# Kernel tuning notes

Hardware: AMD Instinct MI355X
Metric: run time of the kernel (lower is better)

## Reference

```python
import jax, jax.numpy as jnp
import numpy as np

N = 50000      # nodes
E = 800000     # edges (before self-loops)
IN = 128       # in_channels
HID = 32       # hidden_channels
H = 4          # heads (hidden layers)
H_LAST = 6     # heads of final conv (concat=False -> mean)
OUT = 2        # out_channels
NEG = 0.2      # LeakyReLU slope in GATConv


def setup_inputs() -> dict:
    key = jax.random.key(0)
    ks = jax.random.split(key, 24)
    r = lambda k, s, sc=0.1: (jax.random.normal(k, s, jnp.float32) * sc)
    inp = {
        "x": jax.random.normal(ks[0], (N, IN), jnp.float32),
        "edge_index": jax.random.randint(ks[1], (2, E), 0, N, dtype=jnp.int32),
        "edge_attr": jax.random.normal(ks[2], (E, 1), jnp.float32),  # ignored by GATConv (edge_dim=None)
        # layer 0: GATConv(IN -> HID, heads=H, concat) + Linear(IN -> HID*H)
        "c0_W": r(ks[3], (IN, H * HID)), "c0_as": r(ks[4], (H, HID)), "c0_ad": r(ks[5], (H, HID)), "c0_b": jnp.zeros((H * HID,), jnp.float32),
        "l0_W": r(ks[6], (IN, H * HID)), "l0_b": jnp.zeros((H * HID,), jnp.float32),
        # layer 1 (middle): GATConv(HID*H -> HID, heads=H) + Linear(HID*H -> HID*H)
        "c1_W": r(ks[7], (H * HID, H * HID)), "c1_as": r(ks[8], (H, HID)), "c1_ad": r(ks[9], (H, HID)), "c1_b": jnp.zeros((H * HID,), jnp.float32),
        "l1_W": r(ks[10], (H * HID, H * HID)), "l1_b": jnp.zeros((H * HID,), jnp.float32),
        # layer 2 (last): GATConv(HID*H -> OUT, heads=H_LAST, concat=False) + Linear(HID*H -> OUT)
        "c2_W": r(ks[11], (H * HID, H_LAST * OUT)), "c2_as": r(ks[12], (H_LAST, OUT)), "c2_ad": r(ks[13], (H_LAST, OUT)), "c2_b": jnp.zeros((OUT,), jnp.float32),
        "l2_W": r(ks[14], (H * HID, OUT)), "l2_b": jnp.zeros((OUT,), jnp.float32),
    }
    return inp


def gat_conv(x, src, dst, W, a_src, a_dst, b, heads, ch, concat):
    n = x.shape[0]
    xw = (x @ W).reshape(n, heads, ch)                      # [N,H,C]
    al_s = jnp.einsum('nhc,hc->nh', xw, a_src)              # [N,H]
    al_d = jnp.einsum('nhc,hc->nh', xw, a_dst)
    alpha = jax.nn.leaky_relu(al_s[src] + al_d[dst], NEG)   # [E,H]
    # segment softmax over edges sharing the same destination node
    m = jax.ops.segment_max(alpha, dst, num_segments=n)
    e = jnp.exp(alpha - m[dst])
    s = jax.ops.segment_sum(e, dst, num_segments=n)
    coef = e / s[dst]                                       # [E,H]
    out = jax.ops.segment_sum(xw[src] * coef[:, :, None], dst, num_segments=n)  # [N,H,C]
    out = out.reshape(n, heads * ch) if concat else out.mean(axis=1)
    return out + b


def reference(x, edge_index, edge_attr,
              c0_W, c0_as, c0_ad, c0_b, l0_W, l0_b,
              c1_W, c1_as, c1_ad, c1_b, l1_W, l1_b,
              c2_W, c2_as, c2_ad, c2_b, l2_W, l2_b):
    n = x.shape[0]
    loops = jnp.arange(n, dtype=edge_index.dtype)  # GATConv add_self_loops=True
    src = jnp.concatenate([edge_index[0], loops])
    dst = jnp.concatenate([edge_index[1], loops])
    # edge_attr is ignored: GATConv built without edge_dim has lin_edge=None
    h = jax.nn.relu(gat_conv(x, src, dst, c0_W, c0_as, c0_ad, c0_b, H, HID, True) + x @ l0_W + l0_b)
    h = jax.nn.relu(gat_conv(h, src, dst, c1_W, c1_as, c1_ad, c1_b, H, HID, True) + h @ l1_W + l1_b)
    out = gat_conv(h, src, dst, c2_W, c2_as, c2_ad, c2_b, H_LAST, OUT, False) + h @ l2_W + l2_b
    return out
```

## Files before the change

kernel.cpp:

```cpp
#include <hip/hip_runtime.h>
#include <hip/hip_bf16.h>


#define NEG_SLOPE 0.2f
#define SC_CHUNK 4096
#define CAP 64
#define CSTR 16

typedef __attribute__((ext_vector_type(8))) short short8;
typedef __attribute__((ext_vector_type(4))) float floatx4;

static __device__ __forceinline__ float leaky(float x) {
    return x > 0.f ? x : NEG_SLOPE * x;
}

static __device__ __forceinline__ unsigned short f2bf(float f) {
    unsigned int u = __float_as_uint(f);
    u = (u + 0x7fffu + ((u >> 16) & 1u)) >> 16;
    return (unsigned short)u;
}

static __device__ __forceinline__ unsigned int pack_bf2(float lo, float hi) {
    return (unsigned int)f2bf(lo) | ((unsigned int)f2bf(hi) << 16);
}

static __device__ __forceinline__ float bflo(unsigned int u) {
    return __uint_as_float(u << 16);
}
static __device__ __forceinline__ float bfhi(unsigned int u) {
    return __uint_as_float(u & 0xffff0000u);
}

static __device__ __forceinline__ short8 frag_from_f32(const float* p) {
    float4 f0 = ((const float4*)p)[0];
    float4 f1 = ((const float4*)p)[1];
    short8 r;
    r[0] = (short)f2bf(f0.x); r[1] = (short)f2bf(f0.y);
    r[2] = (short)f2bf(f0.z); r[3] = (short)f2bf(f0.w);
    r[4] = (short)f2bf(f1.x); r[5] = (short)f2bf(f1.y);
    r[6] = (short)f2bf(f1.z); r[7] = (short)f2bf(f1.w);
    return r;
}

__global__ __launch_bounds__(256) void k_bucket(
    const int* __restrict__ ei, int E, int N, int rs,
    int* __restrict__ cnt, unsigned short* __restrict__ col,
    const float* __restrict__ W0, unsigned short* __restrict__ T0,
    const float* __restrict__ W1, unsigned short* __restrict__ T1,
    const float* __restrict__ W2, unsigned short* __restrict__ T2,
    const float* __restrict__ W3, unsigned short* __restrict__ T3,
    const float* __restrict__ c2W, const float* __restrict__ l2W,
    unsigned short* __restrict__ WT5) {
    if (blockIdx.y == gridDim.y - 1) {
        int tid = blockIdx.x * 256 + threadIdx.x;
        for (int j = tid; j < 65536; j += 2048) {
            int wsel = j >> 14, t = j & 16383;
            int n = t >> 7, k = t & 127;
            const float* W = (wsel == 0) ? W0 : (wsel == 1) ? W1 : (wsel == 2) ? W2 : W3;
            unsigned short* T = (wsel == 0) ? T0 : (wsel == 1) ? T1 : (wsel == 2) ? T2 : T3;
            T[n * 128 + k] = f2bf(W[k * 128 + n]);
        }
        {
            int n = tid >> 7, k = tid & 127;
            float v = 0.f;
            if (n < 12) v = c2W[k * 12 + n];
            else if (n < 14) v = l2W[k * 2 + (n - 12)];
            WT5[n * 128 + k] = f2bf(v);
        }
        return;
    }
    int lo = blockIdx.x * rs, hi = lo + rs;
    int base = blockIdx.y * SC_CHUNK;
    int ET = E + N;
#pragma unroll 4
    for (int o = threadIdx.x; o < SC_CHUNK; o += 256) {
        int e = base + o;
        if (e >= ET) break;
        int d = (e < E) ? ei[E + e] : (e - E);
        if (d < lo || d >= hi) continue;
        int s = (e < E) ? ei[e] : d;
        int pos = atomicAdd(&cnt[d * CSTR], 1);
        if (pos < CAP) col[(d << 6) + pos] = (unsigned short)s;
    }
}

__global__ __launch_bounds__(256) void k_gemm_mfma(
    const float* __restrict__ x0,
    const unsigned short* __restrict__ Ab,
    const unsigned short* __restrict__ W1T,
    unsigned int* __restrict__ XWb,
    const float* __restrict__ a_s, const float* __restrict__ a_d,
    float4* __restrict__ ALS4, float4* __restrict__ ALD4,
    const unsigned short* __restrict__ W2T,
    const float* __restrict__ b2,
    unsigned short* __restrict__ Hsb,
    int M) {
    __shared__ short8 Wl[128 * 17];
    int which = blockIdx.y;
    const short8* W8 = (const short8*)(which ? W2T : W1T);

    for (int u = threadIdx.x; u < 2048; u += 256)
        Wl[(u >> 4) * 17 + (u & 15)] = W8[u];

    int w = threadIdx.x >> 6, lane = threadIdx.x & 63;
    int m = lane & 15, q = lane >> 4;
    const short8* A8 = (const short8*)Ab;

    short8 af[2][4];
    int rt0 = blockIdx.x * 8 + w;
#pragma unroll
    for (int t = 0; t < 2; t++) {
        int arow = (rt0 + t * 4) * 16 + m;
        int lrow = (arow < M) ? arow : (M - 1);
#pragma unroll
        for (int ks = 0; ks < 4; ks++) {
            af[t][ks] = x0 ? frag_from_f32(x0 + (size_t)lrow * 128 + (ks * 4 + q) * 8)
                           : A8[arow * 16 + ks * 4 + q];
        }
    }
    __syncthreads();

#pragma unroll
    for (int t = 0; t < 2; t++) {
        floatx4 acc[8];
#pragma unroll
        for (int ct = 0; ct < 8; ct++) acc[ct] = (floatx4){0.f, 0.f, 0.f, 0.f};
#pragma unroll
        for (int ks = 0; ks < 4; ks++) {
#pragma unroll
            for (int ct = 0; ct < 8; ct++) {
                short8 bfrag = Wl[(ct * 16 + m) * 17 + ks * 4 + q];
                acc[ct] = __builtin_amdgcn_mfma_f32_16x16x32_bf16(af[t][ks], bfrag, acc[ct], 0, 0, 0);
            }
        }

        int crow0 = (rt0 + t * 4) * 16 + q * 4;
        if (which) {
#pragma unroll
            for (int ct = 0; ct < 8; ct++) {
                int gc = ct * 16 + m;
                float bias = b2[gc];
#pragma unroll
                for (int r = 0; r < 4; r++) {
                    int gr = crow0 + r;
                    if (gr < M) Hsb[gr * 128 + gc] = f2bf(acc[ct][r] + bias);
                }
            }
        } else {
#pragma unroll
            for (int ct = 0; ct < 4; ct++) {
#pragma unroll
                for (int r = 0; r < 4; r++) {
                    int gr = crow0 + r;
                    if (gr < M)
                        XWb[gr * 64 + ct * 16 + m] = pack_bf2(acc[ct][r], acc[ct + 4][r]);
                }
            }
            float sv[4][4], dv[4][4];
#pragma unroll
            for (int h = 0; h < 4; h++) {
                float as0 = a_s[h * 32 + m], as1 = a_s[h * 32 + 16 + m];
                float ad0 = a_d[h * 32 + m], ad1 = a_d[h * 32 + 16 + m];
#pragma unroll
                for (int r = 0; r < 4; r++) {
                    sv[h][r] = acc[2 * h][r] * as0 + acc[2 * h + 1][r] * as1;
                    dv[h][r] = acc[2 * h][r] * ad0 + acc[2 * h + 1][r] * ad1;
                }
            }
#pragma unroll
            for (int off = 8; off >= 1; off >>= 1) {
#pragma unroll
                for (int h = 0; h < 4; h++)
#pragma unroll
                    for (int r = 0; r < 4; r++) {
                        sv[h][r] += __shfl_xor(sv[h][r], off);
                        dv[h][r] += __shfl_xor(dv[h][r], off);
                    }
            }
            if (m == 0) {
#pragma unroll
                for (int r = 0; r < 4; r++) {
                    int gr = crow0 + r;
                    if (gr < M) {
                        ALS4[gr] = make_float4(sv[0][r], sv[1][r], sv[2][r], sv[3][r]);
                        ALD4[gr] = make_float4(dv[0][r], dv[1][r], dv[2][r], dv[3][r]);
                    }
                }
            }
        }
    }
}

__global__ __launch_bounds__(256) void k_gemm_small(
    const unsigned short* __restrict__ Ab,
    const unsigned short* __restrict__ WT5,
    const float* __restrict__ c2as, const float* __restrict__ c2ad,
    const float* __restrict__ l2b,
    float* __restrict__ L2D, float* __restrict__ ALD2,
    float* __restrict__ out, int M) {
    int w = threadIdx.x >> 6, lane = threadIdx.x & 63;
    int m = lane & 15, q = lane >> 4;
    const short8* A8 = (const short8*)Ab;
    const short8* W8 = (const short8*)WT5;
    floatx4 acc = (floatx4){0.f, 0.f, 0.f, 0.f};
    int arow = blockIdx.x * 64 + w * 16 + m;
#pragma unroll
    for (int ks = 0; ks < 4; ks++) {
        short8 afrag = A8[arow * 16 + ks * 4 + q];
        short8 bfrag = W8[m * 16 + ks * 4 + q];
        acc = __builtin_amdgcn_mfma_f32_16x16x32_bf16(afrag, bfrag, acc, 0, 0, 0);
    }
    float asm_ = (m < 12) ? c2as[m] : 0.f;
    float adm  = (m < 12) ? c2ad[m] : 0.f;
    int crow0 = blockIdx.x * 64 + w * 16 + q * 4;
    float sc[4], dc[4];
#pragma unroll
    for (int r = 0; r < 4; r++) {
        sc[r] = acc[r] * asm_;
        dc[r] = acc[r] * adm;
    }
#pragma unroll
    for (int r = 0; r < 4; r++) {
        sc[r] += __shfl_xor(sc[r], 1);
        dc[r] += __shfl_xor(dc[r], 1);
    }
#pragma unroll
    for (int r = 0; r < 4; r++) {
        int gr = crow0 + r;
        if (gr >= M) continue;
        if (m < 12) {
            L2D[gr * 20 + m] = acc[r];
            if ((m & 1) == 0) {
                int h = m >> 1;
                L2D[gr * 20 + 12 + h] = sc[r];
                ALD2[gr * 8 + h] = dc[r];
            }
        } else if (m == 12) {
            out[gr * 2 + 0] = acc[r] + l2b[0];
        } else if (m == 13) {
            out[gr * 2 + 1] = acc[r] + l2b[1];
        }
    }
}

__global__ __launch_bounds__(256) void k_agg4(
    const int* __restrict__ cntv, const unsigned short* __restrict__ col,
    const uint4* __restrict__ XWb4,
    const float4* __restrict__ ALS4, const float4* __restrict__ ALD4,
    const float* __restrict__ cb,
    const unsigned short* __restrict__ Hsb, unsigned short* __restrict__ Hb, int N) {
    int wid = threadIdx.x >> 6, lane = threadIdx.x & 63;
    int node = blockIdx.x * 4 + wid;
    if (node >= N) return;
    int deg = cntv[node * CSTR];
    if (deg > CAP) deg = CAP;
    int start = node << 6;
    int gq = lane >> 4, g = lane & 15;
    int hA = g >> 3;
    int cval = col[start + lane];
    float4 cl = ((const float4*)cb)[g];
    float4 ch = ((const float4*)cb)[g + 16];
    uint2 skl = ((const uint2*)(Hsb + node * 128))[g];
    uint2 skh = ((const uint2*)(Hsb + node * 128 + 64))[g];
    float4 ad = ALD4[node];
    float adA = hA ? ad.y : ad.x;
    float adB = hA ? ad.w : ad.z;

    float a0 = 0.f, a1 = 0.f, a2 = 0.f, a3 = 0.f;
    float b0 = 0.f, b1 = 0.f, b2 = 0.f, b3 = 0.f;
    float sA = 0.f, sB = 0.f;

#define QUAD(qq)                                                        \
    bool t##qq; float4 as##qq; uint4 u##qq;                             \
    {                                                                   \
        int idx = (qq) * 4 + gq;                                        \
        t##qq = idx < deg;                                              \
        int sv = __shfl(cval, t##qq ? idx : 0);                         \
        as##qq = ALS4[sv];                                              \
        u##qq = XWb4[(size_t)sv * 16 + g];                              \
    }

#define CQ(qq)                                                          \
    {                                                                   \
        float eA = t##qq ? __expf(leaky((hA ? as##qq.y : as##qq.x) + adA)) : 0.f; \
        float eB = t##qq ? __expf(leaky((hA ? as##qq.w : as##qq.z) + adB)) : 0.f; \
        sA += eA; sB += eB;                                             \
        a0 += eA * bflo(u##qq.x); b0 += eB * bfhi(u##qq.x);             \
        a1 += eA * bflo(u##qq.y); b1 += eB * bfhi(u##qq.y);             \
        a2 += eA * bflo(u##qq.z); b2 += eB * bfhi(u##qq.z);             \
        a3 += eA * bflo(u##qq.w); b3 += eB * bfhi(u##qq.w);             \
    }

    if (deg <= 16) {
        QUAD(0) QUAD(1) QUAD(2) QUAD(3)
        CQ(0) CQ(1) CQ(2) CQ(3)
    } else if (deg <= 24) {
        QUAD(0) QUAD(1) QUAD(2) QUAD(3) QUAD(4) QUAD(5)
        CQ(0) CQ(1) CQ(2) CQ(3) CQ(4) CQ(5)
    } else {
        QUAD(0) QUAD(1) QUAD(2) QUAD(3) QUAD(4) QUAD(5) QUAD(6) QUAD(7)
        CQ(0) CQ(1) CQ(2) CQ(3) CQ(4) CQ(5) CQ(6) CQ(7)
        for (int i = 32; i < deg; i += 4) {
            int idx = i + gq;
            bool tt = idx < deg;
            int sv = __shfl(cval, tt ? idx : 0);
            float4 as = ALS4[sv];
            uint4 uu = XWb4[(size_t)sv * 16 + g];
            float eA = tt ? __expf(leaky((hA ? as.y : as.x) + adA)) : 0.f;
            float eB = tt ? __expf(leaky((hA ? as.w : as.z) + adB)) : 0.f;
            sA += eA; sB += eB;
            a0 += eA * bflo(uu.x); b0 += eB * bfhi(uu.x);
            a1 += eA * bflo(uu.y); b1 += eB * bfhi(uu.y);
            a2 += eA * bflo(uu.z); b2 += eB * bfhi(uu.z);
            a3 += eA * bflo(uu.w); b3 += eB * bfhi(uu.w);
        }
    }
#undef QUAD
#undef CQ

#define RED2(v) { v += __shfl_xor(v, 16); v += __shfl_xor(v, 32); }
    RED2(sA) RED2(sB)
    RED2(a0) RED2(a1) RED2(a2) RED2(a3)
    RED2(b0) RED2(b1) RED2(b2) RED2(b3)
#undef RED2

    if (gq == 0) {
        float invA = 1.f / sA, invB = 1.f / sB;
        float v0 = a0 * invA + cl.x + bflo(skl.x);
        float v1 = a1 * invA + cl.y + bfhi(skl.x);
        float v2 = a2 * invA + cl.z + bflo(skl.y);
        float v3 = a3 * invA + cl.w + bfhi(skl.y);
        float w0 = b0 * invB + ch.x + bflo(skh.x);
        float w1 = b1 * invB + ch.y + bfhi(skh.x);
        float w2 = b2 * invB + ch.z + bflo(skh.y);
        float w3 = b3 * invB + ch.w + bfhi(skh.y);
        v0 = v0 > 0.f ? v0 : 0.f;  v1 = v1 > 0.f ? v1 : 0.f;
        v2 = v2 > 0.f ? v2 : 0.f;  v3 = v3 > 0.f ? v3 : 0.f;
        w0 = w0 > 0.f ? w0 : 0.f;  w1 = w1 > 0.f ? w1 : 0.f;
        w2 = w2 > 0.f ? w2 : 0.f;  w3 = w3 > 0.f ? w3 : 0.f;
        uint2 ol, oh;
        ol.x = pack_bf2(v0, v1); ol.y = pack_bf2(v2, v3);
        oh.x = pack_bf2(w0, w1); oh.y = pack_bf2(w2, w3);
        ((uint2*)(Hb + node * 128))[g] = ol;
        ((uint2*)(Hb + node * 128 + 64))[g] = oh;
    }
}

__global__ __launch_bounds__(256) void k_agg2(
    const int* __restrict__ cntv, const unsigned short* __restrict__ col,
    const float4* __restrict__ L2D4,
    const float* __restrict__ ALD2,
    const float* __restrict__ c2b,
    float* __restrict__ out, int N) {
    int g = threadIdx.x >> 4, l = threadIdx.x & 15;
    int node = blockIdx.x * 16 + g;
    if (node >= N) return;
    int deg = cntv[node * CSTR];
    if (deg > CAP) deg = CAP;
    int start = node << 6;

    float m0 = (l      < deg) ? 1.f : 0.f;
    float m1 = (l + 16 < deg) ? 1.f : 0.f;
    float m2 = (l + 32 < deg) ? 1.f : 0.f;
    float m3 = (l + 48 < deg) ? 1.f : 0.f;
    int s0 = col[start + ((l      < deg) ? l      : 0)];
    int s1 = col[start + ((l + 16 < deg) ? l + 16 : 0)];
    int s2 = col[start + ((l + 32 < deg) ? l + 32 : 0)];
    int s3 = col[start + ((l + 48 < deg) ? l + 48 : 0)];

    float ald[6];
    {
        float4 d03 = *(const float4*)(ALD2 + node * 8);
        float2 d45 = *(const float2*)(ALD2 + node * 8 + 4);
        ald[0] = d03.x; ald[1] = d03.y; ald[2] = d03.z; ald[3] = d03.w;
        ald[4] = d45.x; ald[5] = d45.y;
    }

#define LOADN(k, sv)                                                       \
    float4 xA##k = L2D4[(size_t)(sv) * 5 + 0];                             \
    float4 xB##k = L2D4[(size_t)(sv) * 5 + 1];                             \
    float4 xC##k = L2D4[(size_t)(sv) * 5 + 2];                             \
    float4 aS##k = L2D4[(size_t)(sv) * 5 + 3];                             \
    float4 aT##k = L2D4[(size_t)(sv) * 5 + 4];
    LOADN(0, s0) LOADN(1, s1) LOADN(2, s2) LOADN(3, s3)
#undef LOADN

    float se[6], a0[6], a1[6];
#pragma unroll
    for (int h = 0; h < 6; h++) { se[h] = 0.f; a0[h] = 0.f; a1[h] = 0.f; }

#define COMPN(k, mk)                                                       \
    {                                                                      \
        float als[6] = {aS##k.x, aS##k.y, aS##k.z, aS##k.w, aT##k.x, aT##k.y}; \
        float xw[12] = {xA##k.x, xA##k.y, xA##k.z, xA##k.w,                \
                        xB##k.x, xB##k.y, xB##k.z, xB##k.w,                \
                        xC##k.x, xC##k.y, xC##k.z, xC##k.w};               \
        _Pragma("unroll")                                                  \
        for (int h = 0; h < 6; h++) {                                      \
            float e = (mk) * __expf(leaky(als[h] + ald[h]));               \
            se[h] += e;                                                    \
            a0[h] += e * xw[2 * h];                                        \
            a1[h] += e * xw[2 * h + 1];                                    \
        }                                                                  \
    }
    COMPN(0, m0) COMPN(1, m1) COMPN(2, m2) COMPN(3, m3)
#undef COMPN

#pragma unroll
    for (int m = 8; m >= 1; m >>= 1) {
#pragma unroll
        for (int h = 0; h < 6; h++) {
            se[h] += __shfl_xor(se[h], m);
            a0[h] += __shfl_xor(a0[h], m);
            a1[h] += __shfl_xor(a1[h], m);
        }
    }
    if (l == 0) {
        float o0 = 0.f, o1 = 0.f;
#pragma unroll
        for (int h = 0; h < 6; h++) {
            float inv = 1.f / se[h];
            o0 += a0[h] * inv;
            o1 += a1[h] * inv;
        }
        out[node * 2 + 0] += o0 * (1.f / 6.f) + c2b[0];
        out[node * 2 + 1] += o1 * (1.f / 6.f) + c2b[1];
    }
}


extern "C" void kernel_launch(void* const* d_in, const int* in_sizes, int n_in,
                              void* d_out, int out_size, void* d_ws, size_t ws_size,
                              hipStream_t stream) {
    const float* x   = (const float*)d_in[0];
    const int* ei    = (const int*)d_in[1];
    const float* c0W = (const float*)d_in[3];
    const float* c0as = (const float*)d_in[4];
    const float* c0ad = (const float*)d_in[5];
    const float* c0b = (const float*)d_in[6];
    const float* l0W = (const float*)d_in[7];
    const float* l0b = (const float*)d_in[8];
    const float* c1W = (const float*)d_in[9];
    const float* c1as = (const float*)d_in[10];
    const float* c1ad = (const float*)d_in[11];
    const float* c1b = (const float*)d_in[12];
    const float* l1W = (const float*)d_in[13];
    const float* l1b = (const float*)d_in[14];
    const float* c2W = (const float*)d_in[15];
    const float* c2as = (const float*)d_in[16];
    const float* c2ad = (const float*)d_in[17];
    const float* c2b = (const float*)d_in[18];
    const float* l2W = (const float*)d_in[19];
    const float* l2b = (const float*)d_in[20];
    float* out = (float*)d_out;

    const int N = in_sizes[0] / 128;
    const int E = in_sizes[1] / 2;
    const int ET = E + N;
    const int Mpad = (N + 63) & ~63;

    char* p = (char*)d_ws;
    auto alloc = [&](size_t bytes) -> void* {
        void* r = (void*)p;
        p += (bytes + 255) & ~(size_t)255;
        return r;
    };
    unsigned short* Hsb = (unsigned short*)alloc((size_t)N * 128 * 2);
    unsigned int* XWb = (unsigned int*)alloc((size_t)N * 64 * 4);
    unsigned short* Ab = (unsigned short*)alloc((size_t)Mpad * 128 * 2);
    unsigned short* W1T = (unsigned short*)alloc(128 * 128 * 2);
    unsigned short* W2T = (unsigned short*)alloc(128 * 128 * 2);
    unsigned short* W3T = (unsigned short*)alloc(128 * 128 * 2);
    unsigned short* W4T = (unsigned short*)alloc(128 * 128 * 2);
    unsigned short* WT5 = (unsigned short*)alloc(16 * 128 * 2);
    float* ALS = (float*)alloc((size_t)N * 4 * 4);
    float* ALD = (float*)alloc((size_t)N * 8 * 4);
    float* L2D = (float*)alloc((size_t)N * 20 * 4);
    int* cnt    = (int*)alloc((size_t)N * CSTR * 4);
    unsigned short* col = (unsigned short*)alloc((size_t)N * CAP * 2);

    hipMemsetAsync(cnt, 0, (size_t)N * CSTR * 4, stream);
    int rs = (N + 7) / 8;
    int chunks = (ET + SC_CHUNK - 1) / SC_CHUNK;
    dim3 bgrid(8, chunks + 1);
    k_bucket<<<bgrid, 256, 0, stream>>>(ei, E, N, rs, cnt, col,
                                        c0W, W1T, l0W, W2T, c1W, W3T, l1W, W4T,
                                        c2W, l2W, WT5);

    dim3 ggrid((Mpad + 127) / 128, 2);
    int nwb = (N + 3) / 4;

    k_gemm_mfma<<<ggrid, 256, 0, stream>>>(x, Ab, W1T, XWb, c0as, c0ad,
                                           (float4*)ALS, (float4*)ALD,
                                           W2T, l0b, Hsb, N);
    k_agg4<<<nwb, 256, 0, stream>>>(cnt, col, (const uint4*)XWb,
                                    (const float4*)ALS, (const float4*)ALD,
                                    c0b, Hsb, Ab, N);

    k_gemm_mfma<<<ggrid, 256, 0, stream>>>(nullptr, Ab, W3T, XWb, c1as, c1ad,
                                           (float4*)ALS, (float4*)ALD,
                                           W4T, l1b, Hsb, N);
    k_agg4<<<nwb, 256, 0, stream>>>(cnt, col, (const uint4*)XWb,
                                    (const float4*)ALS, (const float4*)ALD,
                                    c1b, Hsb, Ab, N);

    k_gemm_small<<<Mpad / 64, 256, 0, stream>>>(Ab, WT5, c2as, c2ad, l2b,
                                                L2D, ALD, out, N);
    k_agg2<<<(N + 15) / 16, 256, 0, stream>>>(cnt, col, (const float4*)L2D,
                                              ALD, c2b, out, N);
}
```

Before: 307.5 us.

## Fuse GAT aggregation with the following layer GEMMs via LDS-staged tiles

Aggregation for layers 0 and 1 now runs inside kernels that also run the next layer's projection. Each block aggregates 64 nodes into a bf16 LDS tile, then feeds that tile straight into MFMA with LDS-cached weights. This removes the global round trip of the aggregated features and two kernel launches. In exchange, each wave now processes 16 nodes one after another and the grid shrinks to 64-node blocks, which cuts the number of waves available to hide gather latency. The attention-logit buffers are split per layer.

```diff
diff --git a/kernel.cpp b/kernel.cpp
--- a/kernel.cpp
+++ b/kernel.cpp
@@ -6,6 +6,7 @@
 #define SC_CHUNK 4096
 #define CAP 64
 #define CSTR 16
+#define HSTR 136
 
 typedef __attribute__((ext_vector_type(8))) short short8;
 typedef __attribute__((ext_vector_type(4))) float floatx4;
@@ -191,78 +192,20 @@
     }
 }
 
-__global__ __launch_bounds__(256) void k_gemm_small(
-    const unsigned short* __restrict__ Ab,
-    const unsigned short* __restrict__ WT5,
-    const float* __restrict__ c2as, const float* __restrict__ c2ad,
-    const float* __restrict__ l2b,
-    float* __restrict__ L2D, float* __restrict__ ALD2,
-    float* __restrict__ out, int M) {
-    int w = threadIdx.x >> 6, lane = threadIdx.x & 63;
-    int m = lane & 15, q = lane >> 4;
-    const short8* A8 = (const short8*)Ab;
-    const short8* W8 = (const short8*)WT5;
-    floatx4 acc = (floatx4){0.f, 0.f, 0.f, 0.f};
-    int arow = blockIdx.x * 64 + w * 16 + m;
-#pragma unroll
-    for (int ks = 0; ks < 4; ks++) {
-        short8 afrag = A8[arow * 16 + ks * 4 + q];
-        short8 bfrag = W8[m * 16 + ks * 4 + q];
-        acc = __builtin_amdgcn_mfma_f32_16x16x32_bf16(afrag, bfrag, acc, 0, 0, 0);
-    }
-    float asm_ = (m < 12) ? c2as[m] : 0.f;
-    float adm  = (m < 12) ? c2ad[m] : 0.f;
-    int crow0 = blockIdx.x * 64 + w * 16 + q * 4;
-    float sc[4], dc[4];
-#pragma unroll
-    for (int r = 0; r < 4; r++) {
-        sc[r] = acc[r] * asm_;
-        dc[r] = acc[r] * adm;
-    }
-#pragma unroll
-    for (int r = 0; r < 4; r++) {
-        sc[r] += __shfl_xor(sc[r], 1);
-        dc[r] += __shfl_xor(dc[r], 1);
-    }
-#pragma unroll
-    for (int r = 0; r < 4; r++) {
-        int gr = crow0 + r;
-        if (gr >= M) continue;
-        if (m < 12) {
-            L2D[gr * 20 + m] = acc[r];
-            if ((m & 1) == 0) {
-                int h = m >> 1;
-                L2D[gr * 20 + 12 + h] = sc[r];
-                ALD2[gr * 8 + h] = dc[r];
-            }
-        } else if (m == 12) {
-            out[gr * 2 + 0] = acc[r] + l2b[0];
-        } else if (m == 13) {
-            out[gr * 2 + 1] = acc[r] + l2b[1];
-        }
-    }
-}
-
-__global__ __launch_bounds__(256) void k_agg4(
-    const int* __restrict__ cntv, const unsigned short* __restrict__ col,
+static __device__ __forceinline__ void agg_node(
+    int deg, const unsigned short* __restrict__ colrow,
     const uint4* __restrict__ XWb4,
-    const float4* __restrict__ ALS4, const float4* __restrict__ ALD4,
+    const float4* __restrict__ ALS4, float4 ad,
     const float* __restrict__ cb,
-    const unsigned short* __restrict__ Hsb, unsigned short* __restrict__ Hb, int N) {
-    int wid = threadIdx.x >> 6, lane = threadIdx.x & 63;
-    int node = blockIdx.x * 4 + wid;
-    if (node >= N) return;
-    int deg = cntv[node * CSTR];
-    if (deg > CAP) deg = CAP;
-    int start = node << 6;
+    const unsigned short* __restrict__ Hsrow,
+    unsigned short* __restrict__ Hrow, int lane) {
     int gq = lane >> 4, g = lane & 15;
     int hA = g >> 3;
-    int cval = col[start + lane];
+    int cval = colrow[lane];
     float4 cl = ((const float4*)cb)[g];
     float4 ch = ((const float4*)cb)[g + 16];
-    uint2 skl = ((const uint2*)(Hsb + node * 128))[g];
-    uint2 skh = ((const uint2*)(Hsb + node * 128 + 64))[g];
-    float4 ad = ALD4[node];
+    uint2 skl = ((const uint2*)Hsrow)[g];
+    uint2 skh = ((const uint2*)(Hsrow + 64))[g];
     float adA = hA ? ad.y : ad.x;
     float adB = hA ? ad.w : ad.z;
 
@@ -341,8 +284,197 @@
         uint2 ol, oh;
         ol.x = pack_bf2(v0, v1); ol.y = pack_bf2(v2, v3);
         oh.x = pack_bf2(w0, w1); oh.y = pack_bf2(w2, w3);
-        ((uint2*)(Hb + node * 128))[g] = ol;
-        ((uint2*)(Hb + node * 128 + 64))[g] = oh;
+        ((uint2*)Hrow)[g] = ol;
+        ((uint2*)(Hrow + 64))[g] = oh;
+    }
+}
+
+__global__ __launch_bounds__(256, 3) void k_fused_ag1(
+    const int* __restrict__ cntv, const unsigned short* __restrict__ col,
+    const uint4* __restrict__ XWb4,
+    const float4* __restrict__ ALS4, const float4* __restrict__ ALD4,
+    const float* __restrict__ c0b, unsigned short* __restrict__ Hsb,
+    const unsigned short* __restrict__ W3T, const unsigned short* __restrict__ W4T,
+    const float* __restrict__ a_s, const float* __restrict__ a_d,
+    const float* __restrict__ l1b,
+    unsigned int* __restrict__ XWb2,
+    float4* __restrict__ ALS2, float4* __restrict__ ALD2,
+    int M) {
+    __shared__ short8 Wl[128 * 17];
+    __shared__ unsigned short Hl[64 * HSTR];
+    int w = threadIdx.x >> 6, lane = threadIdx.x & 63;
+    int r0 = blockIdx.x * 64;
+
+    for (int u = threadIdx.x; u < 2048; u += 256)
+        Wl[(u >> 4) * 17 + (u & 15)] = ((const short8*)W3T)[u];
+
+    for (int i = 0; i < 16; i++) {
+        int node = r0 + i * 4 + w;
+        if (node < M) {
+            int deg = cntv[node * CSTR];
+            if (deg > CAP) deg = CAP;
+            agg_node(deg, col + ((size_t)node << 6), XWb4, ALS4,
+                     ALD4[node], c0b, Hsb + (size_t)node * 128,
+                     Hl + (i * 4 + w) * HSTR, lane);
+        }
+    }
+    __syncthreads();
+
+    int m = lane & 15, q = lane >> 4;
+    short8 af[4];
+#pragma unroll
+    for (int ks = 0; ks < 4; ks++)
+        af[ks] = *(const short8*)(Hl + (w * 16 + m) * HSTR + (ks * 4 + q) * 8);
+
+    int crow0 = r0 + w * 16 + q * 4;
+    {
+        floatx4 acc[8];
+#pragma unroll
+        for (int ct = 0; ct < 8; ct++) acc[ct] = (floatx4){0.f, 0.f, 0.f, 0.f};
+#pragma unroll
+        for (int ks = 0; ks < 4; ks++) {
+#pragma unroll
+            for (int ct = 0; ct < 8; ct++) {
+                short8 bfrag = Wl[(ct * 16 + m) * 17 + ks * 4 + q];
+                acc[ct] = __builtin_amdgcn_mfma_f32_16x16x32_bf16(af[ks], bfrag, acc[ct], 0, 0, 0);
+            }
+        }
+#pragma unroll
+        for (int ct = 0; ct < 4; ct++) {
+#pragma unroll
+            for (int r = 0; r < 4; r++) {
+                int gr = crow0 + r;
+                if (gr < M)
+                    XWb2[gr * 64 + ct * 16 + m] = pack_bf2(acc[ct][r], acc[ct + 4][r]);
+            }
+        }
+        float sv[4][4], dv[4][4];
+#pragma unroll
+        for (int h = 0; h < 4; h++) {
+            float as0 = a_s[h * 32 + m], as1 = a_s[h * 32 + 16 + m];
+            float ad0 = a_d[h * 32 + m], ad1 = a_d[h * 32 + 16 + m];
+#pragma unroll
+            for (int r = 0; r < 4; r++) {
+                sv[h][r] = acc[2 * h][r] * as0 + acc[2 * h + 1][r] * as1;
+                dv[h][r] = acc[2 * h][r] * ad0 + acc[2 * h + 1][r] * ad1;
+            }
+        }
+#pragma unroll
+        for (int off = 8; off >= 1; off >>= 1) {
+#pragma unroll
+            for (int h = 0; h < 4; h++)
+#pragma unroll
+                for (int r = 0; r < 4; r++) {
+                    sv[h][r] += __shfl_xor(sv[h][r], off);
+                    dv[h][r] += __shfl_xor(dv[h][r], off);
+                }
+        }
+        if (m == 0) {
+#pragma unroll
+            for (int r = 0; r < 4; r++) {
+                int gr = crow0 + r;
+                if (gr < M) {
+                    ALS2[gr] = make_float4(sv[0][r], sv[1][r], sv[2][r], sv[3][r]);
+                    ALD2[gr] = make_float4(dv[0][r], dv[1][r], dv[2][r], dv[3][r]);
+                }
+            }
+        }
+    }
+    __syncthreads();
+    for (int u = threadIdx.x; u < 2048; u += 256)
+        Wl[(u >> 4) * 17 + (u & 15)] = ((const short8*)W4T)[u];
+    __syncthreads();
+    {
+        floatx4 acc[8];
+#pragma unroll
+        for (int ct = 0; ct < 8; ct++) acc[ct] = (floatx4){0.f, 0.f, 0.f, 0.f};
+#pragma unroll
+        for (int ks = 0; ks < 4; ks++) {
+#pragma unroll
+            for (int ct = 0; ct < 8; ct++) {
+                short8 bfrag = Wl[(ct * 16 + m) * 17 + ks * 4 + q];
+                acc[ct] = __builtin_amdgcn_mfma_f32_16x16x32_bf16(af[ks], bfrag, acc[ct], 0, 0, 0);
+            }
+        }
+#pragma unroll
+        for (int ct = 0; ct < 8; ct++) {
+            int gc = ct * 16 + m;
+            float bias = l1b[gc];
+#pragma unroll
+            for (int r = 0; r < 4; r++) {
+                int gr = crow0 + r;
+                if (gr < M) Hsb[gr * 128 + gc] = f2bf(acc[ct][r] + bias);
+            }
+        }
+    }
+}
+
+__global__ __launch_bounds__(256) void k_fused_ag2(
+    const int* __restrict__ cntv, const unsigned short* __restrict__ col,
+    const uint4* __restrict__ XWb4,
+    const float4* __restrict__ ALS4, const float4* __restrict__ ALD4,
+    const float* __restrict__ c1b, const unsigned short* __restrict__ Hsb,
+    const unsigned short* __restrict__ WT5,
+    const float* __restrict__ c2as, const float* __restrict__ c2ad,
+    const float* __restrict__ l2b,
+    float* __restrict__ L2D, float* __restrict__ AL2D,
+    float* __restrict__ out, int M) {
+    __shared__ unsigned short Hl[64 * HSTR];
+    int w = threadIdx.x >> 6, lane = threadIdx.x & 63;
+    int r0 = blockIdx.x * 64;
+
+    for (int i = 0; i < 16; i++) {
+        int node = r0 + i * 4 + w;
+        if (node < M) {
+            int deg = cntv[node * CSTR];
+            if (deg > CAP) deg = CAP;
+            agg_node(deg, col + ((size_t)node << 6), XWb4, ALS4,
+                     ALD4[node], c1b, Hsb + (size_t)node * 128,
+                     Hl + (i * 4 + w) * HSTR, lane);
+        }
+    }
+    __syncthreads();
+
+    int m = lane & 15, q = lane >> 4;
+    const short8* W8 = (const short8*)WT5;
+    floatx4 acc = (floatx4){0.f, 0.f, 0.f, 0.f};
+    int rl = w * 16 + m;
+#pragma unroll
+    for (int ks = 0; ks < 4; ks++) {
+        short8 afrag = *(const short8*)(Hl + rl * HSTR + (ks * 4 + q) * 8);
+        short8 bfrag = W8[m * 16 + ks * 4 + q];
+        acc = __builtin_amdgcn_mfma_f32_16x16x32_bf16(afrag, bfrag, acc, 0, 0, 0);
+    }
+    float asm_ = (m < 12) ? c2as[m] : 0.f;
+    float adm  = (m < 12) ? c2ad[m] : 0.f;
+    int crow0 = r0 + w * 16 + q * 4;
+    float sc[4], dc[4];
+#pragma unroll
+    for (int r = 0; r < 4; r++) {
+        sc[r] = acc[r] * asm_;
+        dc[r] = acc[r] * adm;
+    }
+#pragma unroll
+    for (int r = 0; r < 4; r++) {
+        sc[r] += __shfl_xor(sc[r], 1);
+        dc[r] += __shfl_xor(dc[r], 1);
+    }
+#pragma unroll
+    for (int r = 0; r < 4; r++) {
+        int gr = crow0 + r;
+        if (gr >= M) continue;
+        if (m < 12) {
+            L2D[gr * 20 + m] = acc[r];
+            if ((m & 1) == 0) {
+                int h = m >> 1;
+                L2D[gr * 20 + 12 + h] = sc[r];
+                AL2D[gr * 8 + h] = dc[r];
+            }
+        } else if (m == 12) {
+            out[gr * 2 + 0] = acc[r] + l2b[0];
+        } else if (m == 13) {
+            out[gr * 2 + 1] = acc[r] + l2b[1];
+        }
     }
 }
 
@@ -466,16 +598,19 @@
         return r;
     };
     unsigned short* Hsb = (unsigned short*)alloc((size_t)N * 128 * 2);
-    unsigned int* XWb = (unsigned int*)alloc((size_t)N * 64 * 4);
-    unsigned short* Ab = (unsigned short*)alloc((size_t)Mpad * 128 * 2);
+    unsigned int* XWb  = (unsigned int*)alloc((size_t)N * 64 * 4);
+    unsigned int* XWb2 = (unsigned int*)alloc((size_t)N * 64 * 4);
     unsigned short* W1T = (unsigned short*)alloc(128 * 128 * 2);
     unsigned short* W2T = (unsigned short*)alloc(128 * 128 * 2);
     unsigned short* W3T = (unsigned short*)alloc(128 * 128 * 2);
     unsigned short* W4T = (unsigned short*)alloc(128 * 128 * 2);
     unsigned short* WT5 = (unsigned short*)alloc(16 * 128 * 2);
-    float* ALS = (float*)alloc((size_t)N * 4 * 4);
-    float* ALD = (float*)alloc((size_t)N * 8 * 4);
-    float* L2D = (float*)alloc((size_t)N * 20 * 4);
+    float* ALS0 = (float*)alloc((size_t)N * 4 * 4);
+    float* ALD0 = (float*)alloc((size_t)N * 4 * 4);
+    float* ALS1 = (float*)alloc((size_t)N * 4 * 4);
+    float* ALD1 = (float*)alloc((size_t)N * 4 * 4);
+    float* AL2D = (float*)alloc((size_t)N * 8 * 4);
+    float* L2D  = (float*)alloc((size_t)N * 20 * 4);
     int* cnt    = (int*)alloc((size_t)N * CSTR * 4);
     unsigned short* col = (unsigned short*)alloc((size_t)N * CAP * 2);
 
@@ -487,25 +622,22 @@
                                         c0W, W1T, l0W, W2T, c1W, W3T, l1W, W4T,
                                         c2W, l2W, WT5);
 
-    dim3 ggrid((Mpad + 127) / 128, 2);
-    int nwb = (N + 3) / 4;
-
-    k_gemm_mfma<<<ggrid, 256, 0, stream>>>(x, Ab, W1T, XWb, c0as, c0ad,
-                                           (float4*)ALS, (float4*)ALD,
+    int gx = (Mpad + 127) / 128;
+    dim3 ggrid(gx, 2);
+    k_gemm_mfma<<<ggrid, 256, 0, stream>>>(x, nullptr, W1T, XWb, c0as, c0ad,
+                                           (float4*)ALS0, (float4*)ALD0,
                                            W2T, l0b, Hsb, N);
-    k_agg4<<<nwb, 256, 0, stream>>>(cnt, col, (const uint4*)XWb,
-                                    (const float4*)ALS, (const float4*)ALD,
-                                    c0b, Hsb, Ab, N);
-
-    k_gemm_mfma<<<ggrid, 256, 0, stream>>>(nullptr, Ab, W3T, XWb, c1as, c1ad,
-                                           (float4*)ALS, (float4*)ALD,
-                                           W4T, l1b, Hsb, N);
-    k_agg4<<<nwb, 256, 0, stream>>>(cnt, col, (const uint4*)XWb,
-                                    (const float4*)ALS, (const float4*)ALD,
-                                    c1b, Hsb, Ab, N);
-
-    k_gemm_small<<<Mpad / 64, 256, 0, stream>>>(Ab, WT5, c2as, c2ad, l2b,
-                                                L2D, ALD, out, N);
+
+    int nb64 = Mpad / 64;
+    k_fused_ag1<<<nb64, 256, 0, stream>>>(cnt, col, (const uint4*)XWb,
+                                          (const float4*)ALS0, (const float4*)ALD0,
+                                          c0b, Hsb, W3T, W4T, c1as, c1ad, l1b,
+                                          XWb2, (float4*)ALS1, (float4*)ALD1, N);
+    k_fused_ag2<<<nb64, 256, 0, stream>>>(cnt, col, (const uint4*)XWb2,
+                                          (const float4*)ALS1, (const float4*)ALD1,
+                                          c1b, Hsb, WT5, c2as, c2ad, l2b,
+                                          L2D, AL2D, out, N);
+
     k_agg2<<<(N + 15) / 16, 256, 0, stream>>>(cnt, col, (const float4*)L2D,
-                                              ALD, c2b, out, N);
-}
+                                              AL2D, c2b, out, N);
+}
```

Result: slower. 329.9 us (+7.3%).
